# Optimization experiments

Hardware: AMD Instinct MI355X
Metric: run time of the kernel (lower is better)

Reference implementation:

```python
import jax, jax.numpy as jnp
import numpy as np

B, C, H, D, HID = 1024, 64, 64, 256, 256

def setup_inputs() -> dict:
    key = jax.random.key(0)
    k1, k2, k3, k4, k5, k6, k7, k8 = jax.random.split(key, 8)
    candidate_news_vector = jax.random.normal(k1, (B, C, D), dtype=jnp.float32)
    clicked_news_vector = jax.random.normal(k2, (B, H, D), dtype=jnp.float32)
    mask_cand = jax.random.randint(k3, (B, C), 0, 2).astype(bool).at[:, 0].set(True)
    mask_hist = jax.random.randint(k4, (B, H), 0, 2).astype(bool).at[:, 0].set(True)
    # nn.Linear default init: U(-1/sqrt(fan_in), 1/sqrt(fan_in))
    s1 = 1.0 / np.sqrt(2 * D)
    s2 = 1.0 / np.sqrt(HID)
    W1 = jax.random.uniform(k5, (HID, 2 * D), minval=-s1, maxval=s1, dtype=jnp.float32)
    b1 = jax.random.uniform(k6, (HID,), minval=-s1, maxval=s1, dtype=jnp.float32)
    W2 = jax.random.uniform(k7, (1, HID), minval=-s2, maxval=s2, dtype=jnp.float32)
    b2 = jax.random.uniform(k8, (1,), minval=-s2, maxval=s2, dtype=jnp.float32)
    return {"candidate_news_vector": candidate_news_vector,
            "clicked_news_vector": clicked_news_vector,
            "mask_cand": mask_cand, "mask_hist": mask_hist,
            "W1": W1, "b1": b1, "W2": W2, "b2": b2}

def reference(candidate_news_vector, clicked_news_vector, mask_cand, mask_hist, W1, b1, W2, b2):
    d = candidate_news_vector.shape[-1]
    w2 = W2[0]                                  # [HID]
    # Two stacked Linears with no nonlinearity collapse exactly:
    # score = (W2 @ W1_c) . cand + (W2 @ W1_h) . hist + (W2 @ b1 + b2)
    v_c = W1[:, :d].T @ w2                      # [D]
    v_h = W1[:, d:].T @ w2                      # [D]
    bias = jnp.dot(w2, b1) + b2[0]
    scores = (jnp.einsum('bcd,d->bc', candidate_news_vector, v_c)[:, :, None]
              + jnp.einsum('bhd,d->bh', clicked_news_vector, v_h)[:, None, :]
              + bias)                           # [B, C, H]
    neg = jnp.finfo(scores.dtype).min
    scores = jnp.where(mask_hist[:, None, :], scores, neg)
    weights = jax.nn.softmax(scores, axis=-1)   # [B, C, H]
    weights = jnp.where(mask_cand[:, :, None], weights, 0.0)
    user_vector = jnp.einsum('bch,bhd->bcd', weights, clicked_news_vector)
    return user_vector
```

## Files before the change

kernel.cpp:

```cpp
#include <hip/hip_runtime.h>
#include <math.h>

#define NB 1024
#define NC 64
#define NH 64
#define ND 256
#define NHID 256

typedef float f4 __attribute__((ext_vector_type(4)));

#define WS_PART_OFF 1024

__device__ __forceinline__ bool read_mask(const void* m, int idx, int mode) {
  if (mode == 2) return ((const float*)m)[idx] != 0.0f;
  if (mode == 1) return ((const unsigned char*)m)[idx] != 0;
  return ((const int*)m)[idx] != 0;
}

__device__ __forceinline__ void detect_mode(const unsigned int* mask_cand,
                                            const unsigned int* mask_hist,
                                            int* dst) {
  int sawf = 0; unsigned int big = 0;
  for (int i = 0; i < 32; ++i) {
    unsigned int a = mask_hist[i], b = mask_cand[i];
    if (a == 0x3f800000u || b == 0x3f800000u) sawf = 1;
    if ((a > 1u && a != 0x3f800000u) || (b > 1u && b != 0x3f800000u)) big = 1;
  }
  *dst = sawf ? 2 : (big ? 1 : 0);
}

__global__ __launch_bounds__(256) void precompute_p1(
    const float* __restrict__ W1, const float* __restrict__ W2,
    float* __restrict__ ws)
{
  const int g = blockIdx.x;
  const int d = threadIdx.x;
  float acc = 0.f;
  #pragma unroll
  for (int jj = 0; jj < 4; ++jj) {
    int j = g * 4 + jj;
    acc = fmaf(W1[(size_t)j * (2 * ND) + ND + d], W2[j], acc);
  }
  ws[WS_PART_OFF + g * ND + d] = acc;
}

__global__ __launch_bounds__(256) void precompute_p2(
    const unsigned int* __restrict__ mask_cand,
    const unsigned int* __restrict__ mask_hist,
    float* __restrict__ ws)
{
  const int d = threadIdx.x;
  float acc = 0.f;
  #pragma unroll 8
  for (int g = 0; g < 64; ++g) acc += ws[WS_PART_OFF + g * ND + d];
  ws[d] = acc;
  if (d == 0) detect_mode(mask_cand, mask_hist, (int*)ws + ND);
}

__global__ __launch_bounds__(1024) void precompute_fallback(
    const float* __restrict__ W1, const float* __restrict__ W2,
    const unsigned int* __restrict__ mask_cand,
    const unsigned int* __restrict__ mask_hist,
    float* __restrict__ ws)
{
  __shared__ float w2_lds[NHID];
  __shared__ float partial[4][ND];
  int t = threadIdx.x;
  if (t < NHID) w2_lds[t] = W2[t];
  __syncthreads();
  int d = t & (ND - 1);
  int g = t >> 8;
  float acc = 0.f;
  #pragma unroll 8
  for (int j = g * 64; j < g * 64 + 64; ++j)
    acc = fmaf(W1[(size_t)j * (2 * ND) + ND + d], w2_lds[j], acc);
  partial[g][d] = acc;
  __syncthreads();
  if (t < ND)
    ws[t] = partial[0][t] + partial[1][t] + partial[2][t] + partial[3][t];
  if (t == 0) detect_mode(mask_cand, mask_hist, (int*)ws + ND);
}

__global__ __launch_bounds__(512, 8) void user_encoder_kernel(
    const float* __restrict__ hist,
    const void* __restrict__ mask_cand_v,
    const void* __restrict__ mask_hist_v,
    const float* __restrict__ ws,
    float* __restrict__ out)
{
  const int b = blockIdx.x;
  const int t = threadIdx.x;
  const int lane = t & 63;
  const int w = t >> 6;

  __shared__ float s_lds[NH];
  __shared__ float4 part[8][64];

  const int mode = ((const int*)ws)[ND];
  const float4* hb4 = reinterpret_cast<const float4*>(hist + (size_t)b * NH * ND);
  const float4* vh4p = reinterpret_cast<const float4*>(ws);

  {
    const int r = t >> 3, cg = t & 7;
    float p = 0.f;
    #pragma unroll
    for (int i = 0; i < 8; ++i) {
      float4 x = hb4[r * 64 + i * 8 + cg];
      float4 v = vh4p[i * 8 + cg];
      p = fmaf(x.x, v.x, fmaf(x.y, v.y, fmaf(x.z, v.z, fmaf(x.w, v.w, p))));
    }
    p += __shfl_xor(p, 1); p += __shfl_xor(p, 2); p += __shfl_xor(p, 4);
    if (cg == 0)
      s_lds[r] = read_mask(mask_hist_v, b * NH + r, mode) ? p : -3.0e38f;
  }
  __syncthreads();

  float wval;
  {
    float s = s_lds[lane];
    float m = s;
    #pragma unroll
    for (int off = 32; off; off >>= 1) m = fmaxf(m, __shfl_xor(m, off));
    float e = expf(s - m);
    float sum = e;
    #pragma unroll
    for (int off = 32; off; off >>= 1) sum += __shfl_xor(sum, off);
    wval = e / sum;
  }

  {
    float4 acc = {0.f, 0.f, 0.f, 0.f};
    #pragma unroll
    for (int j = 0; j < 8; ++j) {
      float wj = __shfl(wval, (w << 3) | j);
      float4 x = hb4[((w << 3) | j) * 64 + lane];
      acc.x = fmaf(wj, x.x, acc.x);
      acc.y = fmaf(wj, x.y, acc.y);
      acc.z = fmaf(wj, x.z, acc.z);
      acc.w = fmaf(wj, x.w, acc.w);
    }
    part[w][lane] = acc;
  }
  __syncthreads();

  {
    float4 uv = part[0][lane];
    #pragma unroll
    for (int g = 1; g < 8; ++g) {
      float4 q = part[g][lane];
      uv.x += q.x; uv.y += q.y; uv.z += q.z; uv.w += q.w;
    }
    float4* ob4 = reinterpret_cast<float4*>(out + (size_t)b * NC * ND);
    #pragma unroll
    for (int k = 0; k < 8; ++k) {
      int c = w + k * 8;
      bool mc = read_mask(mask_cand_v, b * NC + c, mode);
      f4 val = mc ? (f4){uv.x, uv.y, uv.z, uv.w} : (f4){0.f, 0.f, 0.f, 0.f};
      __builtin_nontemporal_store(val, reinterpret_cast<f4*>(&ob4[c * 64 + lane]));
    }
  }
}

extern "C" void kernel_launch(void* const* d_in, const int* in_sizes, int n_in,
                              void* d_out, int out_size, void* d_ws, size_t ws_size,
                              hipStream_t stream) {
  (void)in_sizes; (void)n_in; (void)out_size;
  const float* hist = (const float*)d_in[1];
  const void*  mask_cand = d_in[2];
  const void*  mask_hist = d_in[3];
  const float* W1 = (const float*)d_in[4];
  const float* W2 = (const float*)d_in[6];
  float* ws = (float*)d_ws;
  float* out = (float*)d_out;

  if (ws_size >= (size_t)(WS_PART_OFF + 64 * ND) * sizeof(float)) {
    precompute_p1<<<64, 256, 0, stream>>>(W1, W2, ws);
    precompute_p2<<<1, 256, 0, stream>>>(
        (const unsigned int*)mask_cand, (const unsigned int*)mask_hist, ws);
  } else {
    precompute_fallback<<<1, 1024, 0, stream>>>(
        W1, W2, (const unsigned int*)mask_cand, (const unsigned int*)mask_hist, ws);
  }
  user_encoder_kernel<<<NB, 512, 0, stream>>>(hist, mask_cand, mask_hist, ws, out);
}
```

Measured before the change: 43.58 us.

## Split user encoder into score/uv kernel and separate broadcast kernel

Splits the fused kernel in two. The first kernel computes the softmax-weighted history vector per batch and writes only that to workspace, or into the first row of the output when workspace is small. A second kernel then broadcasts it to all candidate rows under the candidate mask, spread over more blocks. The aim is to separate the read-bound phase from the write-heavy broadcast so the stores get more parallelism. The cost is an extra launch and a round trip of the intermediate vector through memory.

```diff
diff --git a/kernel.cpp b/kernel.cpp
--- a/kernel.cpp
+++ b/kernel.cpp
@@ -10,6 +10,7 @@
 typedef float f4 __attribute__((ext_vector_type(4)));
 
 #define WS_PART_OFF 1024
+#define WS_UV_OFF   32768
 
 __device__ __forceinline__ bool read_mask(const void* m, int idx, int mode) {
   if (mode == 2) return ((const float*)m)[idx] != 0.0f;
@@ -81,32 +82,32 @@
   if (t == 0) detect_mode(mask_cand, mask_hist, (int*)ws + ND);
 }
 
-__global__ __launch_bounds__(512, 8) void user_encoder_kernel(
+template <int UV_STRIDE>
+__global__ __launch_bounds__(512, 8) void score_uv_kernel(
     const float* __restrict__ hist,
-    const void* __restrict__ mask_cand_v,
     const void* __restrict__ mask_hist_v,
     const float* __restrict__ ws,
-    float* __restrict__ out)
+    float* __restrict__ uv_dst)
 {
   const int b = blockIdx.x;
   const int t = threadIdx.x;
   const int lane = t & 63;
-  const int w = t >> 6;
+  const int g = t >> 6;
 
   __shared__ float s_lds[NH];
-  __shared__ float4 part[8][64];
+  __shared__ f4 part[8][64];
 
   const int mode = ((const int*)ws)[ND];
-  const float4* hb4 = reinterpret_cast<const float4*>(hist + (size_t)b * NH * ND);
-  const float4* vh4p = reinterpret_cast<const float4*>(ws);
+  const f4* hb4 = reinterpret_cast<const f4*>(hist + (size_t)b * NH * ND);
+  const f4* vh4p = reinterpret_cast<const f4*>(ws);
 
   {
     const int r = t >> 3, cg = t & 7;
     float p = 0.f;
     #pragma unroll
     for (int i = 0; i < 8; ++i) {
-      float4 x = hb4[r * 64 + i * 8 + cg];
-      float4 v = vh4p[i * 8 + cg];
+      f4 x = hb4[r * 64 + i * 8 + cg];
+      f4 v = vh4p[i * 8 + cg];
       p = fmaf(x.x, v.x, fmaf(x.y, v.y, fmaf(x.z, v.z, fmaf(x.w, v.w, p))));
     }
     p += __shfl_xor(p, 1); p += __shfl_xor(p, 2); p += __shfl_xor(p, 4);
@@ -129,35 +130,65 @@
   }
 
   {
-    float4 acc = {0.f, 0.f, 0.f, 0.f};
+    f4 acc = {0.f, 0.f, 0.f, 0.f};
     #pragma unroll
     for (int j = 0; j < 8; ++j) {
-      float wj = __shfl(wval, (w << 3) | j);
-      float4 x = hb4[((w << 3) | j) * 64 + lane];
-      acc.x = fmaf(wj, x.x, acc.x);
-      acc.y = fmaf(wj, x.y, acc.y);
-      acc.z = fmaf(wj, x.z, acc.z);
-      acc.w = fmaf(wj, x.w, acc.w);
+      float wj = __shfl(wval, g * 8 + j);
+      f4 x = hb4[(g * 8 + j) * 64 + lane];
+      acc += wj * x;
     }
-    part[w][lane] = acc;
-  }
-  __syncthreads();
-
-  {
-    float4 uv = part[0][lane];
-    #pragma unroll
-    for (int g = 1; g < 8; ++g) {
-      float4 q = part[g][lane];
-      uv.x += q.x; uv.y += q.y; uv.z += q.z; uv.w += q.w;
-    }
-    float4* ob4 = reinterpret_cast<float4*>(out + (size_t)b * NC * ND);
-    #pragma unroll
-    for (int k = 0; k < 8; ++k) {
-      int c = w + k * 8;
-      bool mc = read_mask(mask_cand_v, b * NC + c, mode);
-      f4 val = mc ? (f4){uv.x, uv.y, uv.z, uv.w} : (f4){0.f, 0.f, 0.f, 0.f};
-      __builtin_nontemporal_store(val, reinterpret_cast<f4*>(&ob4[c * 64 + lane]));
-    }
+    part[g][lane] = acc;
+  }
+  __syncthreads();
+
+  if (t < 64) {
+    f4 uv = part[0][t];
+    #pragma unroll
+    for (int q = 1; q < 8; ++q) uv += part[q][t];
+    reinterpret_cast<f4*>(uv_dst + (size_t)b * UV_STRIDE)[t] = uv;
+  }
+}
+
+__global__ __launch_bounds__(256) void broadcast_kernel(
+    const float* __restrict__ uv_src,
+    const void* __restrict__ mask_cand_v,
+    const float* __restrict__ ws,
+    float* __restrict__ out)
+{
+  const int bid = blockIdx.x;
+  const int b = bid >> 2, q = bid & 3;
+  const int t = threadIdx.x, lane = t & 63, g = t >> 6;
+  const int mode = ((const int*)ws)[ND];
+  const f4 uv = reinterpret_cast<const f4*>(uv_src + (size_t)b * ND)[lane];
+  f4* ob4 = reinterpret_cast<f4*>(out + (size_t)b * NC * ND);
+  const f4 zero = {0.f, 0.f, 0.f, 0.f};
+  #pragma unroll
+  for (int j = 0; j < 4; ++j) {
+    int c = q * 16 + g * 4 + j;
+    bool mc = read_mask(mask_cand_v, b * NC + c, mode);
+    f4 val = mc ? uv : zero;
+    __builtin_nontemporal_store(val, &ob4[c * 64 + lane]);
+  }
+}
+
+__global__ __launch_bounds__(256) void broadcast_stash_kernel(
+    const void* __restrict__ mask_cand_v,
+    const float* __restrict__ ws,
+    float* __restrict__ out)
+{
+  const int b = blockIdx.x;
+  const int t = threadIdx.x, lane = t & 63, g = t >> 6;
+  const int mode = ((const int*)ws)[ND];
+  f4* ob4 = reinterpret_cast<f4*>(out + (size_t)b * NC * ND);
+  const f4 uv = reinterpret_cast<const f4*>(ob4)[lane];
+  __syncthreads();
+  const f4 zero = {0.f, 0.f, 0.f, 0.f};
+  #pragma unroll
+  for (int k = 0; k < 16; ++k) {
+    int c = g * 16 + k;
+    bool mc = read_mask(mask_cand_v, b * NC + c, mode);
+    f4 val = mc ? uv : zero;
+    __builtin_nontemporal_store(val, &ob4[c * 64 + lane]);
   }
 }
 
@@ -173,7 +204,10 @@
   float* ws = (float*)d_ws;
   float* out = (float*)d_out;
 
-  if (ws_size >= (size_t)(WS_PART_OFF + 64 * ND) * sizeof(float)) {
+  const bool mid = ws_size >= (size_t)(WS_PART_OFF + 64 * ND) * sizeof(float);
+  const bool big = ws_size >= (size_t)(WS_UV_OFF + NB * ND) * sizeof(float);
+
+  if (mid) {
     precompute_p1<<<64, 256, 0, stream>>>(W1, W2, ws);
     precompute_p2<<<1, 256, 0, stream>>>(
         (const unsigned int*)mask_cand, (const unsigned int*)mask_hist, ws);
@@ -181,5 +215,12 @@
     precompute_fallback<<<1, 1024, 0, stream>>>(
         W1, W2, (const unsigned int*)mask_cand, (const unsigned int*)mask_hist, ws);
   }
-  user_encoder_kernel<<<NB, 512, 0, stream>>>(hist, mask_cand, mask_hist, ws, out);
-}
+
+  if (big) {
+    score_uv_kernel<ND><<<NB, 512, 0, stream>>>(hist, mask_hist, ws, ws + WS_UV_OFF);
+    broadcast_kernel<<<NB * 4, 256, 0, stream>>>(ws + WS_UV_OFF, mask_cand, ws, out);
+  } else {
+    score_uv_kernel<NC * ND><<<NB, 512, 0, stream>>>(hist, mask_hist, ws, out);
+    broadcast_stash_kernel<<<NB, 256, 0, stream>>>(mask_cand, ws, out);
+  }
+}
```

New measurement: 47.76 us. +9.6%, slower.
